# Kernel optimization log

Measured on AMD Instinct MI355X. Metric: run time of the kernel, lower is better.

## Reference

```python
import jax, jax.numpy as jnp
import numpy as np

N_NODES = 50000
N_EDGES = 800000
N_FEAT = 512
HIDDEN = 256
N_CLASSES = 40


def setup_inputs() -> dict:
    key = jax.random.key(0)
    ks = jax.random.split(key, 8)
    x = jax.random.normal(ks[0], (N_NODES, N_FEAT), dtype=jnp.float32)
    edge_src = jax.random.randint(ks[1], (N_EDGES,), 0, N_NODES, dtype=jnp.int32)
    edge_dst = jax.random.randint(ks[2], (N_EDGES,), 0, N_NODES, dtype=jnp.int32)
    edge_w = jax.random.uniform(ks[3], (N_EDGES,), dtype=jnp.float32)
    W1 = jax.random.normal(ks[4], (N_FEAT, HIDDEN), dtype=jnp.float32) * (1.0 / np.sqrt(N_FEAT))
    b1 = jnp.zeros((HIDDEN,), dtype=jnp.float32)
    W2 = jax.random.normal(ks[5], (HIDDEN, N_CLASSES), dtype=jnp.float32) * (1.0 / np.sqrt(HIDDEN))
    b2 = jnp.zeros((N_CLASSES,), dtype=jnp.float32)
    return {"x": x, "edge_src": edge_src, "edge_dst": edge_dst, "edge_w": edge_w,
            "W1": W1, "b1": b1, "W2": W2, "b2": b2}


def _spmm(edge_src, edge_dst, edge_w, h, n_nodes):
    # A_hat @ h with A_hat given as weighted edge list: out[dst] += w * h[src]
    msgs = h[edge_src] * edge_w[:, None]            # [E, d]
    return jax.ops.segment_sum(msgs, edge_dst, num_segments=n_nodes)


def reference(x, edge_src, edge_dst, edge_w, W1, b1, W2, b2):
    n = x.shape[0]
    # Layer 1: relu(A_hat @ (X W1) + b1)
    h = jnp.dot(x, W1)                              # [N, H]
    h = _spmm(edge_src, edge_dst, edge_w, h, n) + b1
    h = jax.nn.relu(h)
    # Layer 2: A_hat @ (H W2) + b2
    z = jnp.dot(h, W2)                              # [N, C]
    z = _spmm(edge_src, edge_dst, edge_w, z, n) + b2
    return jax.nn.log_softmax(z, axis=1)
```

## Files before the change

kernel.cpp:

```cpp
#include <hip/hip_runtime.h>
#include <hip/hip_bf16.h>
#include <stdint.h>

#define N_NODES   50000
#define N_EDGES   800000
#define N_FEAT    512
#define HIDDEN    256
#define N_CLASSES 40
#define NPAD      48
#define SCAN_BLOCKS 196

typedef __attribute__((ext_vector_type(8))) short short8;
typedef __attribute__((ext_vector_type(8))) __bf16 bf16x8;
typedef __attribute__((ext_vector_type(4))) float f32x4;
typedef __attribute__((ext_vector_type(2))) float f32x2;

__device__ inline unsigned short f2bf(float f) {
    unsigned int u = __builtin_bit_cast(unsigned int, f);
    u += 0x7FFFu + ((u >> 16) & 1u);
    return (unsigned short)(u >> 16);
}
__device__ inline float bf2f(unsigned short s) {
    unsigned int u = ((unsigned int)s) << 16;
    return __builtin_bit_cast(float, u);
}

__device__ inline void gload16(const void* g, void* l) {
    typedef __attribute__((address_space(1))) const unsigned int gu32;
    typedef __attribute__((address_space(3))) unsigned int lu32;
    __builtin_amdgcn_global_load_lds((gu32*)g, (lu32*)l, 16, 0, 0);
}

__global__ __launch_bounds__(256) void zero_kernel(int* __restrict__ counts) {
    int i = blockIdx.x * 256 + threadIdx.x;
    if (i < N_NODES) counts[i] = 0;
}

__global__ __launch_bounds__(256) void hist_kernel(const int* __restrict__ edge_dst,
                                                   int* __restrict__ counts,
                                                   int* __restrict__ eoff) {
    int e = blockIdx.x * 256 + threadIdx.x;
    if (e < N_EDGES) eoff[e] = atomicAdd(&counts[edge_dst[e]], 1);
}

__global__ __launch_bounds__(256) void block_sum_kernel(const int* __restrict__ counts,
                                                        int* __restrict__ bsums) {
    int i = blockIdx.x * 256 + threadIdx.x;
    int v = (i < N_NODES) ? counts[i] : 0;
#pragma unroll
    for (int off = 32; off > 0; off >>= 1) v += __shfl_xor(v, off, 64);
    __shared__ int ws[4];
    int lane = threadIdx.x & 63, w = threadIdx.x >> 6;
    if (lane == 0) ws[w] = v;
    __syncthreads();
    if (threadIdx.x == 0) bsums[blockIdx.x] = ws[0] + ws[1] + ws[2] + ws[3];
}

__global__ __launch_bounds__(256) void bsum_scan_kernel(const int* __restrict__ bsums,
                                                        int* __restrict__ boff,
                                                        int* __restrict__ row_ptr) {
    int t = threadIdx.x;
    int lane = t & 63, w = t >> 6;
    int v = (t < SCAN_BLOCKS) ? bsums[t] : 0;
    int inc = v;
#pragma unroll
    for (int off = 1; off < 64; off <<= 1) {
        int u = __shfl_up(inc, off, 64);
        if (lane >= off) inc += u;
    }
    __shared__ int wsum[4];
    if (lane == 63) wsum[w] = inc;
    __syncthreads();
    int add = 0;
    for (int j = 0; j < w; j++) add += wsum[j];
    if (t < SCAN_BLOCKS) boff[t] = add + inc - v;
    if (t == SCAN_BLOCKS - 1) row_ptr[N_NODES] = add + inc;
}

__global__ __launch_bounds__(256) void scan_apply_kernel(const int* __restrict__ counts,
                                                         const int* __restrict__ boff,
                                                         int* __restrict__ row_ptr) {
    int i = blockIdx.x * 256 + threadIdx.x;
    int lane = threadIdx.x & 63, w = threadIdx.x >> 6;
    int v = (i < N_NODES) ? counts[i] : 0;
    int inc = v;
#pragma unroll
    for (int off = 1; off < 64; off <<= 1) {
        int u = __shfl_up(inc, off, 64);
        if (lane >= off) inc += u;
    }
    __shared__ int wsum[4];
    if (lane == 63) wsum[w] = inc;
    __syncthreads();
    int add = 0;
    for (int j = 0; j < w; j++) add += wsum[j];
    if (i < N_NODES) row_ptr[i] = boff[blockIdx.x] + add + inc - v;
}

__global__ __launch_bounds__(256) void scatter_kernel(const int* __restrict__ edge_src,
                                                      const int* __restrict__ edge_dst,
                                                      const float* __restrict__ edge_w,
                                                      const int* __restrict__ rp,
                                                      const int* __restrict__ eoff,
                                                      int2* __restrict__ edge_srt) {
    int e = blockIdx.x * 256 + threadIdx.x;
    if (e >= N_EDGES) return;
    int pos = rp[edge_dst[e]] + eoff[e];
    int2 v;
    v.x = edge_src[e];
    v.y = __float_as_int(edge_w[e]);
    edge_srt[pos] = v;
}

__global__ __launch_bounds__(256) void w1_tcast_kernel(const float* __restrict__ W1,
                                                       unsigned short* __restrict__ W1T) {
    int idx = blockIdx.x * 256 + threadIdx.x;
    int k = idx >> 8, n = idx & 255;
    W1T[(size_t)n * N_FEAT + k] = f2bf(W1[idx]);
}

__global__ __launch_bounds__(256) void w2_tcast_kernel(const float* __restrict__ W2,
                                                       unsigned short* __restrict__ W2T) {
    int idx = blockIdx.x * 256 + threadIdx.x;
    int n = idx >> 8, k = idx & 255;
    float v = (n < N_CLASSES) ? W2[k * N_CLASSES + n] : 0.f;
    W2T[idx] = f2bf(v);
}

__global__ __launch_bounds__(256) void gemm1_mfma(const float* __restrict__ X,
                                                  const unsigned short* __restrict__ W1T,
                                                  unsigned char* __restrict__ T1f8) {
    __shared__ __align__(16) float          As[32 * 64];
    __shared__ __align__(16) unsigned short Bs[256 * 64];
    const int tid  = threadIdx.x;
    const int lane = tid & 63;
    const int w    = tid >> 6;
    const int m0   = blockIdx.x * 32;
    const int l15  = lane & 15;
    const int g    = lane >> 4;
    const int wbase = tid & ~63;

    f32x4 acc[2][4] = {};

    for (int k0 = 0; k0 < N_FEAT; k0 += 64) {
        __syncthreads();
#pragma unroll
        for (int i = 0; i < 2; i++) {
            int slot = i * 256 + tid;
            int row = slot >> 4, c16 = slot & 15;
            int csrc = c16 ^ ((row & 7) << 1);
            int gm = m0 + row;
            if (gm > N_NODES - 1) gm = N_NODES - 1;
            gload16(&X[(size_t)gm * N_FEAT + k0 + csrc * 4],
                    &As[(size_t)(i * 256 + wbase) * 4]);
        }
#pragma unroll
        for (int i = 0; i < 8; i++) {
            int slot = i * 256 + tid;
            int n = slot >> 3, cs = slot & 7;
            int csrc = cs ^ (n & 7);
            gload16(&W1T[(size_t)n * N_FEAT + k0 + csrc * 8],
                    &Bs[(size_t)(i * 256 + wbase) * 8]);
        }
        asm volatile("s_waitcnt vmcnt(0)" ::: "memory");
        __syncthreads();
#pragma unroll
        for (int ko = 0; ko < 2; ko++) {
            int c = ko * 4 + g;
            bf16x8 a[2];
            bf16x8 b[4];
#pragma unroll
            for (int mi = 0; mi < 2; mi++) {
                int row = mi * 16 + l15;
                const float* pa = &As[row * 64 + ((2 * c) ^ ((row & 7) << 1)) * 4];
                float4 v0 = *reinterpret_cast<const float4*>(pa);
                float4 v1 = *reinterpret_cast<const float4*>(pa + 4);
                short8 s;
                s[0] = (short)f2bf(v0.x); s[1] = (short)f2bf(v0.y);
                s[2] = (short)f2bf(v0.z); s[3] = (short)f2bf(v0.w);
                s[4] = (short)f2bf(v1.x); s[5] = (short)f2bf(v1.y);
                s[6] = (short)f2bf(v1.z); s[7] = (short)f2bf(v1.w);
                a[mi] = __builtin_bit_cast(bf16x8, s);
            }
#pragma unroll
            for (int ni = 0; ni < 4; ni++) {
                int n = w * 64 + ni * 16 + l15;
                short8 s = *reinterpret_cast<const short8*>(
                    &Bs[(n * 8 + (c ^ (n & 7))) * 8]);
                b[ni] = __builtin_bit_cast(bf16x8, s);
            }
#pragma unroll
            for (int mi = 0; mi < 2; mi++)
#pragma unroll
                for (int ni = 0; ni < 4; ni++)
                    acc[mi][ni] = __builtin_amdgcn_mfma_f32_16x16x32_bf16(
                        a[mi], b[ni], acc[mi][ni], 0, 0, 0);
        }
    }
#pragma unroll
    for (int mi = 0; mi < 2; mi++) {
#pragma unroll
        for (int r = 0; r < 4; r++) {
            int gm = m0 + mi * 16 + g * 4 + r;
            if (gm < N_NODES) {
#pragma unroll
                for (int ni = 0; ni < 4; ni++) {
                    int n = w * 64 + ni * 16 + l15;
                    int pk = __builtin_amdgcn_cvt_pk_fp8_f32(acc[mi][ni][r],
                                                             acc[mi][ni][r], 0, false);
                    T1f8[(size_t)gm * HIDDEN + n] = (unsigned char)(pk & 0xff);
                }
            }
        }
    }
}

__global__ __launch_bounds__(256) void spmm_relu_kernel(const unsigned char* __restrict__ T1f8,
                                                        const int* __restrict__ rp,
                                                        const int2* __restrict__ edges,
                                                        const float* __restrict__ b1,
                                                        unsigned short* __restrict__ Hout) {
    int node = blockIdx.x * 8 + (threadIdx.x >> 5);
    int lane = threadIdx.x & 31;
    int s = rp[node], e = rp[node + 1];
    const int fo = lane * 8;
    float a[8];
#pragma unroll
    for (int j = 0; j < 8; j++) a[j] = 0.f;
    int i = s;
    for (; i + 3 < e; i += 4) {
        int2 ed[4];
        uint2 p[4];
#pragma unroll
        for (int j = 0; j < 4; j++) ed[j] = edges[i + j];
#pragma unroll
        for (int j = 0; j < 4; j++)
            p[j] = *reinterpret_cast<const uint2*>(&T1f8[(size_t)ed[j].x * HIDDEN + fo]);
#pragma unroll
        for (int j = 0; j < 4; j++) {
            float w = __int_as_float(ed[j].y);
            f32x2 v0 = __builtin_amdgcn_cvt_pk_f32_fp8(p[j].x, false);
            f32x2 v1 = __builtin_amdgcn_cvt_pk_f32_fp8(p[j].x, true);
            f32x2 v2 = __builtin_amdgcn_cvt_pk_f32_fp8(p[j].y, false);
            f32x2 v3 = __builtin_amdgcn_cvt_pk_f32_fp8(p[j].y, true);
            a[0] += w * v0[0]; a[1] += w * v0[1];
            a[2] += w * v1[0]; a[3] += w * v1[1];
            a[4] += w * v2[0]; a[5] += w * v2[1];
            a[6] += w * v3[0]; a[7] += w * v3[1];
        }
    }
    for (; i < e; i++) {
        int2 e0 = edges[i];
        uint2 p0 = *reinterpret_cast<const uint2*>(&T1f8[(size_t)e0.x * HIDDEN + fo]);
        float w = __int_as_float(e0.y);
        f32x2 v0 = __builtin_amdgcn_cvt_pk_f32_fp8(p0.x, false);
        f32x2 v1 = __builtin_amdgcn_cvt_pk_f32_fp8(p0.x, true);
        f32x2 v2 = __builtin_amdgcn_cvt_pk_f32_fp8(p0.y, false);
        f32x2 v3 = __builtin_amdgcn_cvt_pk_f32_fp8(p0.y, true);
        a[0] += w * v0[0]; a[1] += w * v0[1];
        a[2] += w * v1[0]; a[3] += w * v1[1];
        a[4] += w * v2[0]; a[5] += w * v2[1];
        a[6] += w * v3[0]; a[7] += w * v3[1];
    }
    float4 bv0 = *reinterpret_cast<const float4*>(&b1[fo]);
    float4 bv1 = *reinterpret_cast<const float4*>(&b1[fo + 4]);
    a[0] = fmaxf(a[0] + bv0.x, 0.f);
    a[1] = fmaxf(a[1] + bv0.y, 0.f);
    a[2] = fmaxf(a[2] + bv0.z, 0.f);
    a[3] = fmaxf(a[3] + bv0.w, 0.f);
    a[4] = fmaxf(a[4] + bv1.x, 0.f);
    a[5] = fmaxf(a[5] + bv1.y, 0.f);
    a[6] = fmaxf(a[6] + bv1.z, 0.f);
    a[7] = fmaxf(a[7] + bv1.w, 0.f);
    uint4 o;
    o.x = (unsigned int)f2bf(a[0]) | ((unsigned int)f2bf(a[1]) << 16);
    o.y = (unsigned int)f2bf(a[2]) | ((unsigned int)f2bf(a[3]) << 16);
    o.z = (unsigned int)f2bf(a[4]) | ((unsigned int)f2bf(a[5]) << 16);
    o.w = (unsigned int)f2bf(a[6]) | ((unsigned int)f2bf(a[7]) << 16);
    *reinterpret_cast<uint4*>(&Hout[(size_t)node * HIDDEN + fo]) = o;
}

__global__ __launch_bounds__(256) void gemm2_mfma(const unsigned short* __restrict__ Hm,
                                                  const unsigned short* __restrict__ W2T,
                                                  unsigned short* __restrict__ outb) {
    const int tid  = threadIdx.x;
    const int lane = tid & 63;
    const int w    = tid >> 6;
    const int l15  = lane & 15;
    const int g    = lane >> 4;
    const int m0   = blockIdx.x * 64 + w * 16;

    int arow = m0 + l15;
    bool rok = arow < N_NODES;
    const unsigned short* hrow = &Hm[(size_t)arow * HIDDEN];

    f32x4 acc[3] = {};
#pragma unroll
    for (int k0 = 0; k0 < HIDDEN; k0 += 32) {
        bf16x8 a = {};
        if (rok) {
            short8 s = *reinterpret_cast<const short8*>(&hrow[k0 + g * 8]);
            a = __builtin_bit_cast(bf16x8, s);
        }
#pragma unroll
        for (int ni = 0; ni < 3; ni++) {
            short8 s = *reinterpret_cast<const short8*>(
                &W2T[(size_t)(ni * 16 + l15) * HIDDEN + k0 + g * 8]);
            bf16x8 b = __builtin_bit_cast(bf16x8, s);
            acc[ni] = __builtin_amdgcn_mfma_f32_16x16x32_bf16(a, b, acc[ni], 0, 0, 0);
        }
    }
#pragma unroll
    for (int ni = 0; ni < 3; ni++) {
#pragma unroll
        for (int r = 0; r < 4; r++) {
            int m = m0 + g * 4 + r;
            int n = ni * 16 + l15;
            if (m < N_NODES && n < N_CLASSES)
                outb[(size_t)m * N_CLASSES + n] = f2bf(acc[ni][r]);
        }
    }
}

__global__ __launch_bounds__(256) void spmm_lsm_kernel(const unsigned short* __restrict__ T2b,
                                                       const int* __restrict__ rp,
                                                       const int2* __restrict__ edges,
                                                       const float* __restrict__ b2,
                                                       float* __restrict__ out) {
    int d = blockIdx.x * 4 + (threadIdx.x >> 6);
    int c = threadIdx.x & 63;
    bool act = c < N_CLASSES;
    int cc = act ? c : 0;
    int s = rp[d], e = rp[d + 1];
    float a0 = 0.f, a1 = 0.f, a2 = 0.f, a3 = 0.f;
    int i = s;
    for (; i + 7 < e; i += 8) {
        int2 ed[8];
        float v[8];
#pragma unroll
        for (int j = 0; j < 8; j++) ed[j] = edges[i + j];
#pragma unroll
        for (int j = 0; j < 8; j++)
            v[j] = bf2f(T2b[(size_t)ed[j].x * N_CLASSES + cc]);
        a0 += __int_as_float(ed[0].y) * v[0];
        a1 += __int_as_float(ed[1].y) * v[1];
        a2 += __int_as_float(ed[2].y) * v[2];
        a3 += __int_as_float(ed[3].y) * v[3];
        a0 += __int_as_float(ed[4].y) * v[4];
        a1 += __int_as_float(ed[5].y) * v[5];
        a2 += __int_as_float(ed[6].y) * v[6];
        a3 += __int_as_float(ed[7].y) * v[7];
    }
    for (; i < e; i++) {
        int2 e0 = edges[i];
        a0 += __int_as_float(e0.y) * bf2f(T2b[(size_t)e0.x * N_CLASSES + cc]);
    }
    float acc = (a0 + a1) + (a2 + a3);
    float z = act ? (acc + b2[c]) : -3.0e38f;
    float m = z;
#pragma unroll
    for (int off = 32; off > 0; off >>= 1) m = fmaxf(m, __shfl_xor(m, off, 64));
    float p = act ? __expf(z - m) : 0.f;
    float ssum = p;
#pragma unroll
    for (int off = 32; off > 0; off >>= 1) ssum += __shfl_xor(ssum, off, 64);
    if (act) out[(size_t)d * N_CLASSES + c] = z - m - __logf(ssum);
}

extern "C" void kernel_launch(void* const* d_in, const int* in_sizes, int n_in,
                              void* d_out, int out_size, void* d_ws, size_t ws_size,
                              hipStream_t stream) {
    const float* x    = (const float*)d_in[0];
    const int*   esrc = (const int*)d_in[1];
    const int*   edst = (const int*)d_in[2];
    const float* ew   = (const float*)d_in[3];
    const float* W1   = (const float*)d_in[4];
    const float* b1   = (const float*)d_in[5];
    const float* W2   = (const float*)d_in[6];
    const float* b2   = (const float*)d_in[7];
    float* out = (float*)d_out;

    uintptr_t p = (uintptr_t)d_ws;
    auto alloc = [&](size_t bytes) -> void* {
        void* r = (void*)p;
        p += (bytes + 255) & ~(size_t)255;
        return r;
    };
    unsigned char*  t1f8   = (unsigned char*)alloc((size_t)N_NODES * HIDDEN);
    unsigned short* hb     = (unsigned short*)alloc((size_t)N_NODES * HIDDEN * 2);
    int*            counts = (int*)alloc((size_t)N_NODES * 4);
    int*            row_ptr= (int*)alloc((size_t)(N_NODES + 1) * 4);
    int*            eoff   = (int*)alloc((size_t)N_EDGES * 4);
    int2*           edge_srt = (int2*)alloc((size_t)N_EDGES * 8);
    unsigned short* W1Tb   = (unsigned short*)alloc((size_t)HIDDEN * N_FEAT * 2);
    unsigned short* W2Tb   = (unsigned short*)alloc((size_t)NPAD * HIDDEN * 2);
    int*            bsums  = (int*)alloc((size_t)SCAN_BLOCKS * 4);
    int*            boff   = (int*)alloc((size_t)SCAN_BLOCKS * 4);
    unsigned short* t2b = (unsigned short*)t1f8;

    zero_kernel<<<SCAN_BLOCKS, 256, 0, stream>>>(counts);
    hist_kernel<<<(N_EDGES + 255) / 256, 256, 0, stream>>>(edst, counts, eoff);
    block_sum_kernel<<<SCAN_BLOCKS, 256, 0, stream>>>(counts, bsums);
    bsum_scan_kernel<<<1, 256, 0, stream>>>(bsums, boff, row_ptr);
    scan_apply_kernel<<<SCAN_BLOCKS, 256, 0, stream>>>(counts, boff, row_ptr);
    scatter_kernel<<<(N_EDGES + 255) / 256, 256, 0, stream>>>(esrc, edst, ew,
                                                              row_ptr, eoff, edge_srt);
    w1_tcast_kernel<<<(N_FEAT * HIDDEN) / 256, 256, 0, stream>>>(W1, W1Tb);
    w2_tcast_kernel<<<(NPAD * HIDDEN) / 256, 256, 0, stream>>>(W2, W2Tb);

    gemm1_mfma<<<(N_NODES + 31) / 32, 256, 0, stream>>>(x, W1Tb, t1f8);
    spmm_relu_kernel<<<N_NODES / 8, 256, 0, stream>>>(t1f8, row_ptr, edge_srt, b1, hb);

    gemm2_mfma<<<(N_NODES + 63) / 64, 256, 0, stream>>>(hb, W2Tb, t2b);
    spmm_lsm_kernel<<<N_NODES / 4, 256, 0, stream>>>(t2b, row_ptr, edge_srt, b2, out);
}
```

Before: 189.2 us.

## Fuse layer-1 SpMM+ReLU with GEMM2 and double gemm1 row tile

Fuses the second dense GEMM into the SpMM+ReLU kernel. Each block stages its 8 aggregated hidden rows in shared memory, and one wave multiplies them by W2 with MFMA, so the N×256 bf16 hidden matrix is never written to or read back from global memory. Separately, gemm1 now covers 64 rows per block instead of 32, which reuses each W1 tile across more rows. The trade-off is that three of the four waves sit idle during the fused GEMM, half of each 16-row MFMA tile is padding, and gemm1 needs more registers and LDS per block.

```diff
diff --git a/kernel.cpp b/kernel.cpp
--- a/kernel.cpp
+++ b/kernel.cpp
@@ -130,22 +130,22 @@
 __global__ __launch_bounds__(256) void gemm1_mfma(const float* __restrict__ X,
                                                   const unsigned short* __restrict__ W1T,
                                                   unsigned char* __restrict__ T1f8) {
-    __shared__ __align__(16) float          As[32 * 64];
+    __shared__ __align__(16) float          As[64 * 64];
     __shared__ __align__(16) unsigned short Bs[256 * 64];
     const int tid  = threadIdx.x;
     const int lane = tid & 63;
     const int w    = tid >> 6;
-    const int m0   = blockIdx.x * 32;
+    const int m0   = blockIdx.x * 64;
     const int l15  = lane & 15;
     const int g    = lane >> 4;
     const int wbase = tid & ~63;
 
-    f32x4 acc[2][4] = {};
+    f32x4 acc[4][4] = {};
 
     for (int k0 = 0; k0 < N_FEAT; k0 += 64) {
         __syncthreads();
 #pragma unroll
-        for (int i = 0; i < 2; i++) {
+        for (int i = 0; i < 4; i++) {
             int slot = i * 256 + tid;
             int row = slot >> 4, c16 = slot & 15;
             int csrc = c16 ^ ((row & 7) << 1);
@@ -167,10 +167,10 @@
 #pragma unroll
         for (int ko = 0; ko < 2; ko++) {
             int c = ko * 4 + g;
-            bf16x8 a[2];
+            bf16x8 a[4];
             bf16x8 b[4];
 #pragma unroll
-            for (int mi = 0; mi < 2; mi++) {
+            for (int mi = 0; mi < 4; mi++) {
                 int row = mi * 16 + l15;
                 const float* pa = &As[row * 64 + ((2 * c) ^ ((row & 7) << 1)) * 4];
                 float4 v0 = *reinterpret_cast<const float4*>(pa);
@@ -190,7 +190,7 @@
                 b[ni] = __builtin_bit_cast(bf16x8, s);
             }
 #pragma unroll
-            for (int mi = 0; mi < 2; mi++)
+            for (int mi = 0; mi < 4; mi++)
 #pragma unroll
                 for (int ni = 0; ni < 4; ni++)
                     acc[mi][ni] = __builtin_amdgcn_mfma_f32_16x16x32_bf16(
@@ -198,7 +198,7 @@
         }
     }
 #pragma unroll
-    for (int mi = 0; mi < 2; mi++) {
+    for (int mi = 0; mi < 4; mi++) {
 #pragma unroll
         for (int r = 0; r < 4; r++) {
             int gm = m0 + mi * 16 + g * 4 + r;
@@ -215,13 +215,17 @@
     }
 }
 
-__global__ __launch_bounds__(256) void spmm_relu_kernel(const unsigned char* __restrict__ T1f8,
-                                                        const int* __restrict__ rp,
-                                                        const int2* __restrict__ edges,
-                                                        const float* __restrict__ b1,
-                                                        unsigned short* __restrict__ Hout) {
-    int node = blockIdx.x * 8 + (threadIdx.x >> 5);
-    int lane = threadIdx.x & 31;
+__global__ __launch_bounds__(256) void spmm_relu_gemm2_kernel(
+        const unsigned char* __restrict__ T1f8,
+        const int* __restrict__ rp,
+        const int2* __restrict__ edges,
+        const float* __restrict__ b1,
+        const unsigned short* __restrict__ W2T,
+        unsigned short* __restrict__ T2b) {
+    __shared__ __align__(16) unsigned short hs[8][HIDDEN];
+    const int hw = threadIdx.x >> 5;
+    const int node = blockIdx.x * 8 + hw;
+    const int lane = threadIdx.x & 31;
     int s = rp[node], e = rp[node + 1];
     const int fo = lane * 8;
     float a[8];
@@ -277,47 +281,36 @@
     o.y = (unsigned int)f2bf(a[2]) | ((unsigned int)f2bf(a[3]) << 16);
     o.z = (unsigned int)f2bf(a[4]) | ((unsigned int)f2bf(a[5]) << 16);
     o.w = (unsigned int)f2bf(a[6]) | ((unsigned int)f2bf(a[7]) << 16);
-    *reinterpret_cast<uint4*>(&Hout[(size_t)node * HIDDEN + fo]) = o;
-}
-
-__global__ __launch_bounds__(256) void gemm2_mfma(const unsigned short* __restrict__ Hm,
-                                                  const unsigned short* __restrict__ W2T,
-                                                  unsigned short* __restrict__ outb) {
-    const int tid  = threadIdx.x;
-    const int lane = tid & 63;
-    const int w    = tid >> 6;
-    const int l15  = lane & 15;
-    const int g    = lane >> 4;
-    const int m0   = blockIdx.x * 64 + w * 16;
-
-    int arow = m0 + l15;
-    bool rok = arow < N_NODES;
-    const unsigned short* hrow = &Hm[(size_t)arow * HIDDEN];
-
-    f32x4 acc[3] = {};
-#pragma unroll
-    for (int k0 = 0; k0 < HIDDEN; k0 += 32) {
-        bf16x8 a = {};
-        if (rok) {
-            short8 s = *reinterpret_cast<const short8*>(&hrow[k0 + g * 8]);
-            a = __builtin_bit_cast(bf16x8, s);
+    *reinterpret_cast<uint4*>(&hs[hw][fo]) = o;
+    __syncthreads();
+    if (threadIdx.x < 64) {
+        const int l15 = threadIdx.x & 15;
+        const int g = threadIdx.x >> 4;
+        f32x4 acc[3] = {};
+#pragma unroll
+        for (int k0 = 0; k0 < HIDDEN; k0 += 32) {
+            bf16x8 af = {};
+            if (l15 < 8) {
+                short8 sa = *reinterpret_cast<const short8*>(&hs[l15][k0 + g * 8]);
+                af = __builtin_bit_cast(bf16x8, sa);
+            }
+#pragma unroll
+            for (int ni = 0; ni < 3; ni++) {
+                short8 sb = *reinterpret_cast<const short8*>(
+                    &W2T[(size_t)(ni * 16 + l15) * HIDDEN + k0 + g * 8]);
+                bf16x8 bf = __builtin_bit_cast(bf16x8, sb);
+                acc[ni] = __builtin_amdgcn_mfma_f32_16x16x32_bf16(af, bf, acc[ni], 0, 0, 0);
+            }
         }
 #pragma unroll
         for (int ni = 0; ni < 3; ni++) {
-            short8 s = *reinterpret_cast<const short8*>(
-                &W2T[(size_t)(ni * 16 + l15) * HIDDEN + k0 + g * 8]);
-            bf16x8 b = __builtin_bit_cast(bf16x8, s);
-            acc[ni] = __builtin_amdgcn_mfma_f32_16x16x32_bf16(a, b, acc[ni], 0, 0, 0);
-        }
-    }
-#pragma unroll
-    for (int ni = 0; ni < 3; ni++) {
-#pragma unroll
-        for (int r = 0; r < 4; r++) {
-            int m = m0 + g * 4 + r;
-            int n = ni * 16 + l15;
-            if (m < N_NODES && n < N_CLASSES)
-                outb[(size_t)m * N_CLASSES + n] = f2bf(acc[ni][r]);
+#pragma unroll
+            for (int r = 0; r < 4; r++) {
+                int nd = g * 4 + r;
+                int n = ni * 16 + l15;
+                if (nd < 8 && n < N_CLASSES)
+                    T2b[(size_t)(blockIdx.x * 8 + nd) * N_CLASSES + n] = f2bf(acc[ni][r]);
+            }
         }
     }
 }
@@ -387,7 +380,7 @@
         return r;
     };
     unsigned char*  t1f8   = (unsigned char*)alloc((size_t)N_NODES * HIDDEN);
-    unsigned short* hb     = (unsigned short*)alloc((size_t)N_NODES * HIDDEN * 2);
+    unsigned short* t2b    = (unsigned short*)alloc((size_t)N_NODES * N_CLASSES * 2);
     int*            counts = (int*)alloc((size_t)N_NODES * 4);
     int*            row_ptr= (int*)alloc((size_t)(N_NODES + 1) * 4);
     int*            eoff   = (int*)alloc((size_t)N_EDGES * 4);
@@ -396,7 +389,6 @@
     unsigned short* W2Tb   = (unsigned short*)alloc((size_t)NPAD * HIDDEN * 2);
     int*            bsums  = (int*)alloc((size_t)SCAN_BLOCKS * 4);
     int*            boff   = (int*)alloc((size_t)SCAN_BLOCKS * 4);
-    unsigned short* t2b = (unsigned short*)t1f8;
 
     zero_kernel<<<SCAN_BLOCKS, 256, 0, stream>>>(counts);
     hist_kernel<<<(N_EDGES + 255) / 256, 256, 0, stream>>>(edst, counts, eoff);
@@ -408,9 +400,10 @@
     w1_tcast_kernel<<<(N_FEAT * HIDDEN) / 256, 256, 0, stream>>>(W1, W1Tb);
     w2_tcast_kernel<<<(NPAD * HIDDEN) / 256, 256, 0, stream>>>(W2, W2Tb);
 
-    gemm1_mfma<<<(N_NODES + 31) / 32, 256, 0, stream>>>(x, W1Tb, t1f8);
-    spmm_relu_kernel<<<N_NODES / 8, 256, 0, stream>>>(t1f8, row_ptr, edge_srt, b1, hb);
-
-    gemm2_mfma<<<(N_NODES + 63) / 64, 256, 0, stream>>>(hb, W2Tb, t2b);
+    gemm1_mfma<<<(N_NODES + 63) / 64, 256, 0, stream>>>(x, W1Tb, t1f8);
+
+    spmm_relu_gemm2_kernel<<<N_NODES / 8, 256, 0, stream>>>(t1f8, row_ptr, edge_srt,
+                                                            b1, W2Tb, t2b);
+
     spmm_lsm_kernel<<<N_NODES / 4, 256, 0, stream>>>(t2b, row_ptr, edge_srt, b2, out);
 }
```

Measured after the change: 192.4 us. No clear change (+1.7%).
